# Kernel tuning notes

Hardware: AMD Instinct MI355X
Metric: run time of the kernel (lower is better)

## Reference

```python
import jax, jax.numpy as jnp
import numpy as np

B, L, D, H, DK, DV = 2, 2048, 1024, 16, 64, 64
NEG_INF = -100000000.0


def setup_inputs() -> dict:
    key = jax.random.key(0)
    ks = jax.random.split(key, 10)
    s = 0.02
    inp = {
        "q": jax.random.normal(ks[0], (B, L, D), jnp.float32),
        "k": jax.random.normal(ks[1], (B, L, D), jnp.float32),
        "v": jax.random.normal(ks[2], (B, L, D), jnp.float32),
        "Wq": jax.random.normal(ks[3], (D, H * DK), jnp.float32) * s,
        "bq": jnp.zeros((H * DK,), jnp.float32),
        "Wk": jax.random.normal(ks[4], (D, H * DK), jnp.float32) * s,
        "bk": jnp.zeros((H * DK,), jnp.float32),
        "Wv": jax.random.normal(ks[5], (D, H * DV), jnp.float32) * s,
        "bv": jnp.zeros((H * DV,), jnp.float32),
        "W0": jax.random.normal(ks[6], (H * DV, D), jnp.float32) * s,
        "b0": jnp.zeros((D,), jnp.float32),
        "key_padding_mask": jax.random.uniform(ks[7], (B, L)) < 0.1,
        # 3D causal mask (B, Lq, Lk); True = masked
        "attn_mask": jnp.broadcast_to(jnp.triu(jnp.ones((L, L), bool), k=1), (B, L, L)),
    }
    return inp


def reference(q, k, v, Wq, bq, Wk, bk, Wv, bv, W0, b0, key_padding_mask, attn_mask):
    b, lq, _ = q.shape
    lk = k.shape[1]
    dk = Wq.shape[1] // H
    dv = Wv.shape[1] // H
    qh = (q @ Wq + bq).reshape(b, lq, H, dk)  # (B,Lq,H,dk)
    kh = (k @ Wk + bk).reshape(b, lk, H, dk)
    vh = (v @ Wv + bv).reshape(b, lk, H, dv)
    # scaled scores (B,H,Lq,Lk)
    attn = jnp.einsum("bqhd,bkhd->bhqk", qh, kh) / jnp.sqrt(jnp.float32(dk))
    # attn_mask (B,Lq,Lk): masked_fill semantics
    attn = jnp.where(attn_mask[:, None, :, :], NEG_INF, attn)
    # key_padding_mask (B,Lq): masks full query rows (broadcast over keys)
    attn = jnp.where(key_padding_mask[:, None, :, None], NEG_INF, attn)
    attn = jax.nn.softmax(attn, axis=-1)
    out = jnp.einsum("bhqk,bkhd->bqhd", attn, vh).reshape(b, lq, H * dv)
    out = out @ W0 + b0  # (B,Lq,D)
    return out, attn
```

## Files before the change

### kernel.cpp

```cpp
#include <hip/hip_runtime.h>

#define B_ 2
#define L_ 2048
#define D_ 1024
#define H_ 16
#define DKV 64
#define NEG_INF -1e8f

typedef float f32x4 __attribute__((ext_vector_type(4)));
typedef __bf16 bf16x8 __attribute__((ext_vector_type(8)));
typedef unsigned int u32x4 __attribute__((ext_vector_type(4)));
typedef unsigned int u32x2 __attribute__((ext_vector_type(2)));
typedef unsigned short u16x4 __attribute__((ext_vector_type(4)));

__device__ __forceinline__ unsigned short f2bfbits(float f) {
  unsigned int u = __builtin_bit_cast(unsigned int, f);
  unsigned int r = (u + 0x7FFFu + ((u >> 16) & 1u)) >> 16;
  return (unsigned short)r;
}
__device__ __forceinline__ float bf2f(unsigned short b) {
  unsigned int u = ((unsigned int)b) << 16;
  return __builtin_bit_cast(float, u);
}

__global__ __launch_bounds__(256) void prep_k(
    const float* __restrict__ xq, const float* __restrict__ xk, const float* __restrict__ xv,
    const float* __restrict__ Wq, const float* __restrict__ Wk,
    const float* __restrict__ Wv, const float* __restrict__ W0,
    const void* __restrict__ kpm_raw,
    unsigned short* __restrict__ oq, unsigned short* __restrict__ ok, unsigned short* __restrict__ ov,
    unsigned short* __restrict__ Wtq, unsigned short* __restrict__ Wtk,
    unsigned short* __restrict__ Wtv, unsigned short* __restrict__ W0t,
    unsigned char* __restrict__ kpmn)
{
  __shared__ float Tl[64][65];
  const int bid = blockIdx.x, tid = threadIdx.x;
  if (bid < 6144) {
    const int proj = bid >> 11;
    const float* X = proj == 0 ? xq : (proj == 1 ? xk : xv);
    unsigned short* O = proj == 0 ? oq : (proj == 1 ? ok : ov);
    const long i8 = ((long)(bid & 2047) * 256 + tid) * 8;
    f32x4 a = *(const f32x4*)(X + i8);
    f32x4 b = *(const f32x4*)(X + i8 + 4);
    u32x4 p;
    p[0] = (unsigned)f2bfbits(a[0]) | ((unsigned)f2bfbits(a[1]) << 16);
    p[1] = (unsigned)f2bfbits(a[2]) | ((unsigned)f2bfbits(a[3]) << 16);
    p[2] = (unsigned)f2bfbits(b[0]) | ((unsigned)f2bfbits(b[1]) << 16);
    p[3] = (unsigned)f2bfbits(b[2]) | ((unsigned)f2bfbits(b[3]) << 16);
    *(u32x4*)(O + i8) = p;
  } else if (bid < 7168) {
    const int wid = bid - 6144;
    const int m = wid >> 8, t = wid & 255;
    const float* W = m == 0 ? Wq : (m == 1 ? Wk : (m == 2 ? Wv : W0));
    unsigned short* Wt = m == 0 ? Wtq : (m == 1 ? Wtk : (m == 2 ? Wtv : W0t));
    const int k0 = ((t >> 4) & 15) * 64, n0 = (t & 15) * 64;
    #pragma unroll
    for (int it = 0; it < 4; ++it) {
      int idx = it * 256 + tid;
      int r = idx >> 4, c4 = (idx & 15) << 2;
      f32x4 x = *(const f32x4*)(W + (long)(k0 + r) * 1024 + n0 + c4);
      Tl[r][c4] = x[0]; Tl[r][c4 + 1] = x[1]; Tl[r][c4 + 2] = x[2]; Tl[r][c4 + 3] = x[3];
    }
    __syncthreads();
    #pragma unroll
    for (int it = 0; it < 2; ++it) {
      int idx = it * 256 + tid;
      int n = idx >> 3, c8 = (idx & 7) << 3;
      u32x4 p;
      #pragma unroll
      for (int j = 0; j < 4; ++j)
        p[j] = (unsigned)f2bfbits(Tl[c8 + 2 * j][n]) | ((unsigned)f2bfbits(Tl[c8 + 2 * j + 1][n]) << 16);
      *(u32x4*)(Wt + (long)(n0 + n) * 1024 + k0 + c8) = p;
    }
  } else {
    __shared__ int flag;
    if (tid == 0) flag = 0;
    __syncthreads();
    const unsigned* w = (const unsigned*)kpm_raw;
    unsigned bad = 0;
    for (int i = tid; i < 1024; i += 256) bad |= (w[i] > 1u) ? 1u : 0u;
    if (bad) flag = 1;
    __syncthreads();
    const bool u8 = (flag != 0);
    const unsigned char* u = (const unsigned char*)kpm_raw;
    for (int i = tid; i < B_ * L_; i += 256)
      kpmn[i] = u8 ? (u[i] != 0) : (w[i] != 0);
  }
}

__global__ __launch_bounds__(256) void colsum_part_k(const unsigned short* __restrict__ vh,
                                                     float* __restrict__ part) {
  __shared__ float red[4][64];
  const int bid = blockIdx.x, tid = threadIdx.x;
  const int z = bid >> 3, seg = bid & 7;
  const int col = tid & 63, rgrp = tid >> 6;
  const long zoff = (long)z * L_ * DKV;
  float s = 0.f;
  #pragma unroll 4
  for (int i = 0; i < 64; ++i) {
    int r = seg * 256 + rgrp + 4 * i;
    s += bf2f(vh[zoff + (long)r * DKV + col]);
  }
  red[rgrp][col] = s;
  __syncthreads();
  if (tid < 64)
    part[(long)bid * 64 + tid] = red[0][tid] + red[1][tid] + red[2][tid] + red[3][tid];
}

__global__ __launch_bounds__(64) void colsum_final_k(const float* __restrict__ part,
                                                     float* __restrict__ colsumV) {
  const int z = blockIdx.x, col = threadIdx.x;
  float s = 0.f;
  #pragma unroll
  for (int seg = 0; seg < 8; ++seg) s += part[((long)z * 8 + seg) * 64 + col];
  colsumV[z * DKV + col] = s;
}

__global__ __launch_bounds__(256) void qkv_gemm_k(
    const unsigned short* __restrict__ xqb, const unsigned short* __restrict__ xkb,
    const unsigned short* __restrict__ xvb,
    const unsigned short* __restrict__ Wtq, const unsigned short* __restrict__ Wtk,
    const unsigned short* __restrict__ Wtv,
    const float* __restrict__ bq, const float* __restrict__ bk, const float* __restrict__ bv,
    unsigned short* __restrict__ oq, unsigned short* __restrict__ ok, unsigned short* __restrict__ ov)
{
  __shared__ __align__(16) unsigned short Al[128][72];
  __shared__ __align__(16) unsigned short Bl[128][72];
  const int proj = blockIdx.y;
  const unsigned short* X  = proj == 0 ? xqb : (proj == 1 ? xkb : xvb);
  const unsigned short* Wt = proj == 0 ? Wtq : (proj == 1 ? Wtk : Wtv);
  const float* bias = proj == 0 ? bq : (proj == 1 ? bk : bv);
  unsigned short* O = proj == 0 ? oq : (proj == 1 ? ok : ov);
  const int mt = blockIdx.x, zp = blockIdx.z;
  const int bb = zp >> 3, hp = zp & 7;
  const int tid = threadIdx.x, lane = tid & 63, w = tid >> 6, g = lane >> 4, l16 = lane & 15;
  const int wm = w >> 1, wn = w & 1;
  const long arow0 = (long)bb * L_ + mt * 128;
  const long brow0 = (long)hp * 128;

  const f32x4 zero4 = {0.f, 0.f, 0.f, 0.f};
  f32x4 acc[4][4];
  #pragma unroll
  for (int i = 0; i < 4; ++i)
    #pragma unroll
    for (int j = 0; j < 4; ++j) acc[i][j] = zero4;

  for (int kt = 0; kt < D_; kt += 64) {
    #pragma unroll
    for (int it = 0; it < 4; ++it) {
      int idx = it * 256 + tid;
      int r = idx >> 3, c8 = (idx & 7) << 3;
      *(u32x4*)&Al[r][c8] = *(const u32x4*)(X + (arow0 + r) * D_ + kt + c8);
      *(u32x4*)&Bl[r][c8] = *(const u32x4*)(Wt + (brow0 + r) * D_ + kt + c8);
    }
    __syncthreads();
    #pragma unroll
    for (int ks = 0; ks < 2; ++ks) {
      bf16x8 a[4], bv8[4];
      #pragma unroll
      for (int fm = 0; fm < 4; ++fm)
        a[fm] = *(const bf16x8*)&Al[wm * 64 + fm * 16 + l16][ks * 32 + g * 8];
      #pragma unroll
      for (int fn = 0; fn < 4; ++fn)
        bv8[fn] = *(const bf16x8*)&Bl[wn * 64 + fn * 16 + l16][ks * 32 + g * 8];
      #pragma unroll
      for (int fm = 0; fm < 4; ++fm)
        #pragma unroll
        for (int fn = 0; fn < 4; ++fn)
          acc[fm][fn] = __builtin_amdgcn_mfma_f32_16x16x32_bf16(a[fm], bv8[fn], acc[fm][fn], 0, 0, 0);
    }
    __syncthreads();
  }
  #pragma unroll
  for (int fm = 0; fm < 4; ++fm)
    #pragma unroll
    for (int fn = 0; fn < 4; ++fn)
      #pragma unroll
      for (int r = 0; r < 4; ++r) {
        int row = mt * 128 + wm * 64 + fm * 16 + g * 4 + r;
        int col = wn * 64 + fn * 16 + l16;
        float val = acc[fm][fn][r] + bias[hp * 128 + col];
        int zh = bb * H_ + hp * 2 + (col >> 6);
        O[(long)zh * L_ * 64 + (long)row * 64 + (col & 63)] = f2bfbits(val);
      }
}

__global__ __launch_bounds__(256) void oproj_gemm_k(
    const unsigned short* __restrict__ Ab, const unsigned short* __restrict__ W0t,
    const float* __restrict__ b0, float* __restrict__ out)
{
  __shared__ __align__(16) unsigned short Al[64][72];
  __shared__ __align__(16) unsigned short Bl[128][72];
  const int mt = blockIdx.x, nt = blockIdx.y;
  const int tid = threadIdx.x, lane = tid & 63, w = tid >> 6, g = lane >> 4, l16 = lane & 15;
  const int wm = w >> 1, wn = w & 1;

  const f32x4 zero4 = {0.f, 0.f, 0.f, 0.f};
  f32x4 acc[2][4];
  #pragma unroll
  for (int i = 0; i < 2; ++i)
    #pragma unroll
    for (int j = 0; j < 4; ++j) acc[i][j] = zero4;

  for (int kt = 0; kt < D_; kt += 64) {
    #pragma unroll
    for (int it = 0; it < 2; ++it) {
      int idx = it * 256 + tid;
      int r = idx >> 3, c8 = (idx & 7) << 3;
      *(u32x4*)&Al[r][c8] = *(const u32x4*)(Ab + (long)(mt * 64 + r) * D_ + kt + c8);
    }
    #pragma unroll
    for (int it = 0; it < 4; ++it) {
      int idx = it * 256 + tid;
      int r = idx >> 3, c8 = (idx & 7) << 3;
      *(u32x4*)&Bl[r][c8] = *(const u32x4*)(W0t + (long)(nt * 128 + r) * D_ + kt + c8);
    }
    __syncthreads();
    #pragma unroll
    for (int ks = 0; ks < 2; ++ks) {
      bf16x8 a[2], bv8[4];
      #pragma unroll
      for (int fm = 0; fm < 2; ++fm)
        a[fm] = *(const bf16x8*)&Al[wm * 32 + fm * 16 + l16][ks * 32 + g * 8];
      #pragma unroll
      for (int fn = 0; fn < 4; ++fn)
        bv8[fn] = *(const bf16x8*)&Bl[wn * 64 + fn * 16 + l16][ks * 32 + g * 8];
      #pragma unroll
      for (int fm = 0; fm < 2; ++fm)
        #pragma unroll
        for (int fn = 0; fn < 4; ++fn)
          acc[fm][fn] = __builtin_amdgcn_mfma_f32_16x16x32_bf16(a[fm], bv8[fn], acc[fm][fn], 0, 0, 0);
    }
    __syncthreads();
  }
  #pragma unroll
  for (int fm = 0; fm < 2; ++fm)
    #pragma unroll
    for (int fn = 0; fn < 4; ++fn)
      #pragma unroll
      for (int r = 0; r < 4; ++r) {
        int row = mt * 64 + wm * 32 + fm * 16 + g * 4 + r;
        int col = nt * 128 + wn * 64 + fn * 16 + l16;
        out[(long)row * D_ + col] = acc[fm][fn][r] + b0[col];
      }
}

__global__ __launch_bounds__(256, 4) void attn_pv_k(
    const unsigned short* __restrict__ qh, const unsigned short* __restrict__ kh,
    const unsigned short* __restrict__ vh, const unsigned char* __restrict__ kpm,
    const float* __restrict__ colsumV, float* __restrict__ attn,
    unsigned short* __restrict__ oh)
{
  __shared__ __align__(16) char smem[64 * 68 * 4];
  auto Ql = (unsigned short (*)[72])smem;
  auto Pl = (float (*)[68])smem;
  __shared__ __align__(16) unsigned short Kl[64][72];
  __shared__ __align__(16) unsigned short Vl[64][72];
  __shared__ unsigned char padl[64];

  const int tid = threadIdx.x, lane = tid & 63, w = tid >> 6, g = lane >> 4, l16 = lane & 15;
  const int bid = blockIdx.x;
  const int z = bid & 31;
  const int sx = bid >> 5;
  const int q0 = sx * 64;
  const int b = z >> 4, h = z & 15;
  const long zoff = (long)z * L_ * DKV;
  const int rowbase = q0 + w * 16 + g * 4;

  const int kr = tid >> 3, kc8 = (tid & 7) << 3;
  const int vk = tid >> 4, vn4 = (tid & 15) << 2;

  #pragma unroll
  for (int it = 0; it < 2; ++it) {
    int f = it * 256 + tid;
    int r = f >> 3, c8 = (f & 7) << 3;
    *(u32x4*)&Ql[r][c8] = *(const u32x4*)(qh + zoff + (long)(q0 + r) * 64 + c8);
  }
  if (tid < 64) padl[tid] = kpm[b * L_ + q0 + tid];
  __syncthreads();
  bf16x8 a[2];
  #pragma unroll
  for (int ks = 0; ks < 2; ++ks)
    a[ks] = *(const bf16x8*)&Ql[w * 16 + l16][ks * 32 + g * 8];
  bool pad[4];
  #pragma unroll
  for (int r = 0; r < 4; ++r) pad[r] = padl[w * 16 + g * 4 + r] != 0;
  __syncthreads();

  const float invL = 1.0f / (float)L_;

  for (int kt = sx + 1; kt < L_ / 64; ++kt) {
    #pragma unroll
    for (int it = 0; it < 4; ++it) {
      int f = it * 256 + tid;
      int r = f >> 4, c4 = (f & 15) << 2;
      float vvv = padl[r] ? invL : 0.f;
      f32x4 ov = {vvv, vvv, vvv, vvv};
      __builtin_nontemporal_store(ov, (f32x4*)&attn[((long)z * L_ + q0 + r) * L_ + kt * 64 + c4]);
    }
  }

  float psum[4] = {0.f, 0.f, 0.f, 0.f};
  const f32x4 zero4 = {0.f, 0.f, 0.f, 0.f};
  f32x4 o[4];
  #pragma unroll
  for (int fn = 0; fn < 4; ++fn) o[fn] = zero4;

  u32x4 Kreg[2];
  u16x4 Vreg[4];
  #pragma unroll
  for (int it = 0; it < 2; ++it)
    Kreg[it] = *(const u32x4*)(kh + zoff + (long)(kr + it * 32) * 64 + kc8);
  #pragma unroll
  for (int it = 0; it < 4; ++it)
    Vreg[it] = *(const u16x4*)(vh + zoff + (long)(vk + it * 16) * 64 + vn4);

  for (int kt = 0; kt <= sx; ++kt) {
    #pragma unroll
    for (int it = 0; it < 2; ++it)
      *(u32x4*)&Kl[kr + it * 32][kc8] = Kreg[it];
    #pragma unroll
    for (int it = 0; it < 4; ++it) {
      int kk = vk + it * 16;
      int sw = kk ^ (((vn4 >> 2) & 7) << 3);
      Vl[vn4 + 0][sw] = Vreg[it][0]; Vl[vn4 + 1][sw] = Vreg[it][1];
      Vl[vn4 + 2][sw] = Vreg[it][2]; Vl[vn4 + 3][sw] = Vreg[it][3];
    }
    __syncthreads();
    if (kt < sx) {
      const long noff = zoff + (long)((kt + 1) * 64) * 64;
      #pragma unroll
      for (int it = 0; it < 2; ++it)
        Kreg[it] = *(const u32x4*)(kh + noff + (long)(kr + it * 32) * 64 + kc8);
      #pragma unroll
      for (int it = 0; it < 4; ++it)
        Vreg[it] = *(const u16x4*)(vh + noff + (long)(vk + it * 16) * 64 + vn4);
    }
    f32x4 s[4];
    #pragma unroll
    for (int fn = 0; fn < 4; ++fn) {
      bf16x8 bv0 = *(const bf16x8*)&Kl[fn * 16 + l16][g * 8];
      bf16x8 bv1 = *(const bf16x8*)&Kl[fn * 16 + l16][32 + g * 8];
      f32x4 t = zero4;
      t = __builtin_amdgcn_mfma_f32_16x16x32_bf16(a[0], bv0, t, 0, 0, 0);
      t = __builtin_amdgcn_mfma_f32_16x16x32_bf16(a[1], bv1, t, 0, 0, 0);
      s[fn] = t;
    }
    #pragma unroll
    for (int fn = 0; fn < 4; ++fn)
      #pragma unroll
      for (int r = 0; r < 4; ++r) {
        int kk = kt * 64 + fn * 16 + l16;
        float sv = s[fn][r] * 0.125f;
        if (kk > rowbase + r) sv = NEG_INF;
        float p = __expf(sv - 12.0f);
        psum[r] += p;
        Pl[w * 16 + g * 4 + r][fn * 16 + l16] = p;
      }
    bf16x8 pa[2];
    #pragma unroll
    for (int ks = 0; ks < 2; ++ks) {
      f32x4 lo = *(const f32x4*)&Pl[w * 16 + l16][ks * 32 + g * 8];
      f32x4 hi = *(const f32x4*)&Pl[w * 16 + l16][ks * 32 + g * 8 + 4];
      bf16x8 t;
      #pragma unroll
      for (int i = 0; i < 4; ++i) { t[i] = (__bf16)lo[i]; t[i + 4] = (__bf16)hi[i]; }
      pa[ks] = t;
    }
    #pragma unroll
    for (int fn = 0; fn < 4; ++fn) {
      int dv = fn * 16 + l16;
      int swz = ((dv >> 2) & 7) << 3;
      bf16x8 vb0 = *(const bf16x8*)&Vl[dv][(0 * 32 + g * 8) ^ swz];
      bf16x8 vb1 = *(const bf16x8*)&Vl[dv][(1 * 32 + g * 8) ^ swz];
      o[fn] = __builtin_amdgcn_mfma_f32_16x16x32_bf16(pa[0], vb0, o[fn], 0, 0, 0);
      o[fn] = __builtin_amdgcn_mfma_f32_16x16x32_bf16(pa[1], vb1, o[fn], 0, 0, 0);
    }
    __syncthreads();
  }

  float linv[4];
  #pragma unroll
  for (int r = 0; r < 4; ++r) {
    float s = psum[r];
    #pragma unroll
    for (int d = 1; d < 16; d <<= 1) s += __shfl_xor(s, d);
    linv[r] = 1.f / s;
  }

  #pragma unroll
  for (int fn = 0; fn < 4; ++fn)
    #pragma unroll
    for (int r = 0; r < 4; ++r) {
      int qq = rowbase + r;
      int dv = fn * 16 + l16;
      float val = pad[r] ? invL * colsumV[z * DKV + dv] : o[fn][r] * linv[r];
      oh[((long)b * L_ + qq) * (H_ * DKV) + h * DKV + dv] = f2bfbits(val);
    }

  u32x4 K2reg[2];
  #pragma unroll
  for (int it = 0; it < 2; ++it)
    Kreg[it] = *(const u32x4*)(kh + zoff + (long)(kr + it * 32) * 64 + kc8);
  if (1 <= sx)
    #pragma unroll
    for (int it = 0; it < 2; ++it)
      K2reg[it] = *(const u32x4*)(kh + zoff + (long)(64 + kr + it * 32) * 64 + kc8);

  for (int kt = 0; kt <= sx; kt += 2) {
    const bool has2 = (kt + 1 <= sx);
    #pragma unroll
    for (int it = 0; it < 2; ++it)
      *(u32x4*)&Kl[kr + it * 32][kc8] = Kreg[it];
    if (has2)
      #pragma unroll
      for (int it = 0; it < 2; ++it)
        *(u32x4*)&Vl[kr + it * 32][kc8] = K2reg[it];
    __syncthreads();
    if (kt + 2 <= sx) {
      const long noff = zoff + (long)((kt + 2) * 64) * 64;
      #pragma unroll
      for (int it = 0; it < 2; ++it)
        Kreg[it] = *(const u32x4*)(kh + noff + (long)(kr + it * 32) * 64 + kc8);
      if (kt + 3 <= sx)
        #pragma unroll
        for (int it = 0; it < 2; ++it)
          K2reg[it] = *(const u32x4*)(kh + noff + (long)(64 + kr + it * 32) * 64 + kc8);
    }
    #pragma unroll
    for (int fn = 0; fn < 4; ++fn) {
      bf16x8 bv0 = *(const bf16x8*)&Kl[fn * 16 + l16][g * 8];
      bf16x8 bv1 = *(const bf16x8*)&Kl[fn * 16 + l16][32 + g * 8];
      f32x4 t = zero4;
      t = __builtin_amdgcn_mfma_f32_16x16x32_bf16(a[0], bv0, t, 0, 0, 0);
      t = __builtin_amdgcn_mfma_f32_16x16x32_bf16(a[1], bv1, t, 0, 0, 0);
      #pragma unroll
      for (int r = 0; r < 4; ++r) {
        int kk = kt * 64 + fn * 16 + l16;
        float sv = t[r] * 0.125f;
        if (kk > rowbase + r) sv = NEG_INF;
        float p = pad[r] ? invL : __expf(sv - 12.0f) * linv[r];
        Pl[w * 16 + g * 4 + r][fn * 16 + l16] = p;
      }
    }
    __syncthreads();
    #pragma unroll
    for (int it = 0; it < 4; ++it) {
      int f = it * 256 + tid;
      int r = f >> 4, c4 = (f & 15) << 2;
      f32x4 ov = *(const f32x4*)&Pl[r][c4];
      __builtin_nontemporal_store(ov, (f32x4*)&attn[((long)z * L_ + q0 + r) * L_ + kt * 64 + c4]);
    }
    if (has2) {
      __syncthreads();
      #pragma unroll
      for (int fn = 0; fn < 4; ++fn) {
        bf16x8 bv0 = *(const bf16x8*)&Vl[fn * 16 + l16][g * 8];
        bf16x8 bv1 = *(const bf16x8*)&Vl[fn * 16 + l16][32 + g * 8];
        f32x4 t = zero4;
        t = __builtin_amdgcn_mfma_f32_16x16x32_bf16(a[0], bv0, t, 0, 0, 0);
        t = __builtin_amdgcn_mfma_f32_16x16x32_bf16(a[1], bv1, t, 0, 0, 0);
        #pragma unroll
        for (int r = 0; r < 4; ++r) {
          int kk = (kt + 1) * 64 + fn * 16 + l16;
          float sv = t[r] * 0.125f;
          if (kk > rowbase + r) sv = NEG_INF;
          float p = pad[r] ? invL : __expf(sv - 12.0f) * linv[r];
          Pl[w * 16 + g * 4 + r][fn * 16 + l16] = p;
        }
      }
      __syncthreads();
      #pragma unroll
      for (int it = 0; it < 4; ++it) {
        int f = it * 256 + tid;
        int r = f >> 4, c4 = (f & 15) << 2;
        f32x4 ov = *(const f32x4*)&Pl[r][c4];
        __builtin_nontemporal_store(ov, (f32x4*)&attn[((long)z * L_ + q0 + r) * L_ + (kt + 1) * 64 + c4]);
      }
    }
  }
}

extern "C" void kernel_launch(void* const* d_in, const int* in_sizes, int n_in,
                              void* d_out, int out_size, void* d_ws, size_t ws_size,
                              hipStream_t stream) {
  (void)in_sizes; (void)n_in; (void)out_size; (void)ws_size;
  const float* q  = (const float*)d_in[0];
  const float* k  = (const float*)d_in[1];
  const float* v  = (const float*)d_in[2];
  const float* Wq = (const float*)d_in[3];
  const float* bq = (const float*)d_in[4];
  const float* Wk = (const float*)d_in[5];
  const float* bk = (const float*)d_in[6];
  const float* Wv = (const float*)d_in[7];
  const float* bv = (const float*)d_in[8];
  const float* W0 = (const float*)d_in[9];
  const float* b0 = (const float*)d_in[10];
  const void*  kpm_raw = d_in[11];

  float* out  = (float*)d_out;
  float* attn = out + (long)B_ * L_ * D_;

  const long XE = (long)B_ * L_ * D_;
  const long HEAD_ELEMS = (long)B_ * H_ * L_ * DKV;
  unsigned short* qh  = (unsigned short*)d_ws;
  unsigned short* kh  = qh + HEAD_ELEMS;
  unsigned short* vh  = kh + HEAD_ELEMS;
  unsigned short* xqb = vh + HEAD_ELEMS;
  unsigned short* xkb = xqb + XE;
  unsigned short* xvb = xkb + XE;
  unsigned short* oh  = xqb;
  unsigned short* Wtq = xvb + XE;
  unsigned short* Wtk = Wtq + (long)D_ * D_;
  unsigned short* Wtv = Wtk + (long)D_ * D_;
  unsigned short* W0t = Wtv + (long)D_ * D_;
  float* colsumV = (float*)(W0t + (long)D_ * D_);
  float* part    = colsumV + 32 * 64;
  unsigned char* kpmn = (unsigned char*)(part + 256 * 64);

  dim3 blk(256);

  prep_k<<<dim3(7169), blk, 0, stream>>>(
      q, k, v, Wq, Wk, Wv, W0, kpm_raw,
      xqb, xkb, xvb, Wtq, Wtk, Wtv, W0t, kpmn);

  qkv_gemm_k<<<dim3(L_ / 128, 3, B_ * (H_ / 2)), blk, 0, stream>>>(
      xqb, xkb, xvb, Wtq, Wtk, Wtv, bq, bk, bv, qh, kh, vh);

  colsum_part_k<<<dim3(256), blk, 0, stream>>>(vh, part);
  colsum_final_k<<<dim3(32), dim3(64), 0, stream>>>(part, colsumV);

  attn_pv_k<<<dim3(1024), blk, 0, stream>>>(
      qh, kh, vh, kpmn, colsumV, attn, oh);

  oproj_gemm_k<<<dim3(B_ * L_ / 64, D_ / 128), blk, 0, stream>>>(
      oh, W0t, b0, out);
}
```

Baseline: 248.0 us.

## Use direct global-to-LDS loads with XOR swizzle in GEMMs and reorder attention blocks

The QKV and output-projection GEMMs now stage tiles with global_load_lds (direct global-to-LDS DMA), replacing loads through registers. The unpadded LDS tiles use an XOR swizzle on 16-byte chunks to avoid bank conflicts, and the fragment reads apply the same swizzle. The attention kernel remaps query-tile indices so causal work is more evenly spread across the launch order. This removes register staging and VGPR pressure but depends on the lane-to-LDS layout of the builtin being exactly right.

```diff
diff --git a/kernel.cpp b/kernel.cpp
--- a/kernel.cpp
+++ b/kernel.cpp
@@ -21,6 +21,12 @@
 __device__ __forceinline__ float bf2f(unsigned short b) {
   unsigned int u = ((unsigned int)b) << 16;
   return __builtin_bit_cast(float, u);
+}
+
+__device__ __forceinline__ void gload16(const unsigned short* g, unsigned short* l) {
+  __builtin_amdgcn_global_load_lds(
+      (const __attribute__((address_space(1))) unsigned int*)g,
+      (__attribute__((address_space(3))) unsigned int*)l, 16, 0, 0);
 }
 
 __global__ __launch_bounds__(256) void prep_k(
@@ -124,8 +130,8 @@
     const float* __restrict__ bq, const float* __restrict__ bk, const float* __restrict__ bv,
     unsigned short* __restrict__ oq, unsigned short* __restrict__ ok, unsigned short* __restrict__ ov)
 {
-  __shared__ __align__(16) unsigned short Al[128][72];
-  __shared__ __align__(16) unsigned short Bl[128][72];
+  __shared__ __align__(16) unsigned short Al[128][64];
+  __shared__ __align__(16) unsigned short Bl[128][64];
   const int proj = blockIdx.y;
   const unsigned short* X  = proj == 0 ? xqb : (proj == 1 ? xkb : xvb);
   const unsigned short* Wt = proj == 0 ? Wtq : (proj == 1 ? Wtk : Wtv);
@@ -137,6 +143,7 @@
   const int wm = w >> 1, wn = w & 1;
   const long arow0 = (long)bb * L_ + mt * 128;
   const long brow0 = (long)hp * 128;
+  const int lr8 = lane >> 3, lc = lane & 7;
 
   const f32x4 zero4 = {0.f, 0.f, 0.f, 0.f};
   f32x4 acc[4][4];
@@ -147,22 +154,25 @@
 
   for (int kt = 0; kt < D_; kt += 64) {
     #pragma unroll
-    for (int it = 0; it < 4; ++it) {
-      int idx = it * 256 + tid;
-      int r = idx >> 3, c8 = (idx & 7) << 3;
-      *(u32x4*)&Al[r][c8] = *(const u32x4*)(X + (arow0 + r) * D_ + kt + c8);
-      *(u32x4*)&Bl[r][c8] = *(const u32x4*)(Wt + (brow0 + r) * D_ + kt + c8);
+    for (int i = 0; i < 4; ++i) {
+      int r = w * 32 + i * 8 + lr8;
+      gload16(X + (arow0 + r) * D_ + kt + ((lc ^ (r & 7)) << 3), &Al[w * 32 + i * 8][0]);
+      gload16(Wt + (brow0 + r) * D_ + kt + ((lc ^ (r & 7)) << 3), &Bl[w * 32 + i * 8][0]);
     }
     __syncthreads();
     #pragma unroll
     for (int ks = 0; ks < 2; ++ks) {
       bf16x8 a[4], bv8[4];
       #pragma unroll
-      for (int fm = 0; fm < 4; ++fm)
-        a[fm] = *(const bf16x8*)&Al[wm * 64 + fm * 16 + l16][ks * 32 + g * 8];
-      #pragma unroll
-      for (int fn = 0; fn < 4; ++fn)
-        bv8[fn] = *(const bf16x8*)&Bl[wn * 64 + fn * 16 + l16][ks * 32 + g * 8];
+      for (int fm = 0; fm < 4; ++fm) {
+        int ra = wm * 64 + fm * 16 + l16;
+        a[fm] = *(const bf16x8*)&Al[ra][((ks * 4 + g) ^ (ra & 7)) << 3];
+      }
+      #pragma unroll
+      for (int fn = 0; fn < 4; ++fn) {
+        int rb = wn * 64 + fn * 16 + l16;
+        bv8[fn] = *(const bf16x8*)&Bl[rb][((ks * 4 + g) ^ (rb & 7)) << 3];
+      }
       #pragma unroll
       for (int fm = 0; fm < 4; ++fm)
         #pragma unroll
@@ -189,11 +199,12 @@
     const unsigned short* __restrict__ Ab, const unsigned short* __restrict__ W0t,
     const float* __restrict__ b0, float* __restrict__ out)
 {
-  __shared__ __align__(16) unsigned short Al[64][72];
-  __shared__ __align__(16) unsigned short Bl[128][72];
+  __shared__ __align__(16) unsigned short Al[64][64];
+  __shared__ __align__(16) unsigned short Bl[128][64];
   const int mt = blockIdx.x, nt = blockIdx.y;
   const int tid = threadIdx.x, lane = tid & 63, w = tid >> 6, g = lane >> 4, l16 = lane & 15;
   const int wm = w >> 1, wn = w & 1;
+  const int lr8 = lane >> 3, lc = lane & 7;
 
   const f32x4 zero4 = {0.f, 0.f, 0.f, 0.f};
   f32x4 acc[2][4];
@@ -204,27 +215,29 @@
 
   for (int kt = 0; kt < D_; kt += 64) {
     #pragma unroll
-    for (int it = 0; it < 2; ++it) {
-      int idx = it * 256 + tid;
-      int r = idx >> 3, c8 = (idx & 7) << 3;
-      *(u32x4*)&Al[r][c8] = *(const u32x4*)(Ab + (long)(mt * 64 + r) * D_ + kt + c8);
-    }
-    #pragma unroll
-    for (int it = 0; it < 4; ++it) {
-      int idx = it * 256 + tid;
-      int r = idx >> 3, c8 = (idx & 7) << 3;
-      *(u32x4*)&Bl[r][c8] = *(const u32x4*)(W0t + (long)(nt * 128 + r) * D_ + kt + c8);
+    for (int i = 0; i < 2; ++i) {
+      int r = w * 16 + i * 8 + lr8;
+      gload16(Ab + (long)(mt * 64 + r) * D_ + kt + ((lc ^ (r & 7)) << 3), &Al[w * 16 + i * 8][0]);
+    }
+    #pragma unroll
+    for (int i = 0; i < 4; ++i) {
+      int r = w * 32 + i * 8 + lr8;
+      gload16(W0t + (long)(nt * 128 + r) * D_ + kt + ((lc ^ (r & 7)) << 3), &Bl[w * 32 + i * 8][0]);
     }
     __syncthreads();
     #pragma unroll
     for (int ks = 0; ks < 2; ++ks) {
       bf16x8 a[2], bv8[4];
       #pragma unroll
-      for (int fm = 0; fm < 2; ++fm)
-        a[fm] = *(const bf16x8*)&Al[wm * 32 + fm * 16 + l16][ks * 32 + g * 8];
-      #pragma unroll
-      for (int fn = 0; fn < 4; ++fn)
-        bv8[fn] = *(const bf16x8*)&Bl[wn * 64 + fn * 16 + l16][ks * 32 + g * 8];
+      for (int fm = 0; fm < 2; ++fm) {
+        int ra = wm * 32 + fm * 16 + l16;
+        a[fm] = *(const bf16x8*)&Al[ra][((ks * 4 + g) ^ (ra & 7)) << 3];
+      }
+      #pragma unroll
+      for (int fn = 0; fn < 4; ++fn) {
+        int rb = wn * 64 + fn * 16 + l16;
+        bv8[fn] = *(const bf16x8*)&Bl[rb][((ks * 4 + g) ^ (rb & 7)) << 3];
+      }
       #pragma unroll
       for (int fm = 0; fm < 2; ++fm)
         #pragma unroll
@@ -261,7 +274,8 @@
   const int tid = threadIdx.x, lane = tid & 63, w = tid >> 6, g = lane >> 4, l16 = lane & 15;
   const int bid = blockIdx.x;
   const int z = bid & 31;
-  const int sx = bid >> 5;
+  const int qq5 = bid >> 5;
+  const int sx = (qq5 & 8) ? ((qq5 & 16) ? 55 - qq5 : 23 - qq5) : qq5;
   const int q0 = sx * 64;
   const int b = z >> 4, h = z & 15;
   const long zoff = (long)z * L_ * DKV;
```

After: 244.3 us. Within noise of the previous version (-1.5%).
